# Kernel tuning notes

Hardware: AMD Instinct MI355X
Metric: run time of the kernel (lower is better)

Reference implementation:

```python
import jax, jax.numpy as jnp
import numpy as np

E = 8      # num_experts
K = 2      # top_k
D = 512    # model dim
H = 2048   # expert hidden dim (4*dim)
EPS = 1e-6


def _rmsnorm(x, w):
    # x: [..., H], w broadcastable to x
    return x * jax.lax.rsqrt(jnp.mean(x * x, axis=-1, keepdims=True) + EPS) * w


def setup_inputs() -> dict:
    key = jax.random.key(0)
    ks = jax.random.split(key, 5)
    B, T = 4, 2048
    x = jax.random.normal(ks[0], (B, T, D), dtype=jnp.float32)
    gate_w = jax.random.normal(ks[1], (D, E), dtype=jnp.float32) / np.sqrt(D)
    w1 = jax.random.normal(ks[2], (E, D, H), dtype=jnp.float32) / np.sqrt(D)
    w2 = jax.random.normal(ks[3], (E, H, H), dtype=jnp.float32) / np.sqrt(H)
    w3 = jax.random.normal(ks[4], (E, H, D), dtype=jnp.float32) / np.sqrt(H)
    n1 = jnp.ones((E, H), dtype=jnp.float32)
    n2 = jnp.ones((E, H), dtype=jnp.float32)
    return {"x": x, "gate_w": gate_w, "w1": w1, "w2": w2, "w3": w3, "n1": n1, "n2": n2}


def reference(x, gate_w, w1, w2, w3, n1, n2):
    B, T, Dm = x.shape
    xf = x.reshape(-1, Dm)                              # [N, D]
    logits = xf @ gate_w                                # [N, E]
    tk_logits, tk_idx = jax.lax.top_k(logits, K)        # [N, K]
    gates = jax.nn.softmax(tk_logits, axis=-1)          # [N, K]

    # Dense compute of all experts (naive MoE, as in the original module).
    h1 = jax.nn.gelu(jnp.einsum('nd,edh->enh', xf, w1), approximate=False)
    h1 = _rmsnorm(h1, n1[:, None, :])                   # [E, N, H]
    h2 = jax.nn.gelu(jnp.einsum('enh,ehk->enk', h1, w2), approximate=False)
    h2 = _rmsnorm(h2, n2[:, None, :])                   # [E, N, H]
    # dropout is identity in eval mode
    expert_out = jnp.einsum('enh,ehd->ned', h2 + h1, w3)  # [N, E, D]

    sel = jnp.take_along_axis(expert_out, tk_idx[:, :, None], axis=1)  # [N, K, D]
    out = jnp.sum(gates[:, :, None] * sel, axis=1)       # [N, D]
    return out.reshape(B, T, Dm)
```

## Files before the change

### kernel.cpp

```cpp
#include <hip/hip_runtime.h>
#include <hip/hip_bf16.h>

using bf16 = __hip_bfloat16;
using short8 = __attribute__((ext_vector_type(8))) short;
using float4v = __attribute__((ext_vector_type(4))) float;

#define N_TOK 8192
#define DMODEL 512
#define HDIM 2048
#define NEXP 8
#define NPAIR 16384
#define PAIR_PAD 16512
#define NGBLK 2048

#define ASYNC_CP16(gsrc, ldst)                                                   \
    __builtin_amdgcn_global_load_lds(                                            \
        (const __attribute__((address_space(1))) void*)(gsrc),                   \
        (__attribute__((address_space(3))) void*)(ldst), 16, 0, 0)

typedef __attribute__((address_space(3))) char lds3_t;

#define BAR() asm volatile("s_barrier" ::: "memory")
#define WAIT_VM4() asm volatile("s_waitcnt vmcnt(4)" ::: "memory")
#define WAIT_VM0() asm volatile("s_waitcnt vmcnt(0)" ::: "memory")
#define SBAR() __builtin_amdgcn_sched_barrier(0)
#define WAITL_(n) asm volatile("s_waitcnt lgkmcnt(" #n ")" ::: "memory")
#define WAITL(n) WAITL_(n)
#define DSR(dst, addr, imm) \
    asm volatile("ds_read_b128 %0, %1 offset:%2" : "=v"(dst) : "v"(addr), "i"(imm))

__device__ __forceinline__ float gelu_fast(float v) {
    float u = v * (0.7978845608f + 0.0356774081f * v * v);
    float t = __expf(-2.0f * u);
    return v * __builtin_amdgcn_rcpf(1.0f + t);
}
__device__ __forceinline__ float bf2f(short s) {
    return __uint_as_float(((unsigned)(unsigned short)s) << 16);
}
__device__ __forceinline__ short f2bf(float f) {
    return (short)__bfloat16_as_ushort(__float2bfloat16(f));
}

__global__ void cvt_x_k(const float* __restrict__ x, bf16* __restrict__ xb) {
    int i = blockIdx.x * 256 + threadIdx.x;
    if (i >= N_TOK * DMODEL / 4) return;
    const float4 f = *(const float4*)(x + (size_t)i * 4);
    union { ushort u[4]; uint2 v; } r;
    r.u[0] = __bfloat16_as_ushort(__float2bfloat16(f.x));
    r.u[1] = __bfloat16_as_ushort(__float2bfloat16(f.y));
    r.u[2] = __bfloat16_as_ushort(__float2bfloat16(f.z));
    r.u[3] = __bfloat16_as_ushort(__float2bfloat16(f.w));
    *(uint2*)(xb + (size_t)i * 4) = r.v;
}

__global__ void gating_k(const float* __restrict__ x, const float* __restrict__ gw,
                         int* __restrict__ tok_idx, float* __restrict__ tok_gate,
                         int* __restrict__ blkc) {
    __shared__ int hist[8];
    if (threadIdx.x < 8) hist[threadIdx.x] = 0;
    __syncthreads();
    int n = blockIdx.x * 4 + (threadIdx.x >> 6);
    int lane = threadIdx.x & 63;
    double acc[NEXP];
#pragma unroll
    for (int e = 0; e < NEXP; e++) acc[e] = 0.0;
    const float* xr = x + (size_t)n * DMODEL;
    for (int d = lane; d < DMODEL; d += 64) {
        float xv = xr[d];
        const float* g = gw + (size_t)d * NEXP;
#pragma unroll
        for (int e = 0; e < NEXP; e++) acc[e] += (double)xv * (double)g[e];
    }
#pragma unroll
    for (int m = 32; m >= 1; m >>= 1)
#pragma unroll
        for (int e = 0; e < NEXP; e++) acc[e] += __shfl_xor(acc[e], m, 64);
    if (lane == 0) {
        double best = acc[0]; int bi = 0;
#pragma unroll
        for (int e = 1; e < NEXP; e++) if (acc[e] > best) { best = acc[e]; bi = e; }
        double best2 = -1e300; int bi2 = 0;
#pragma unroll
        for (int e = 0; e < NEXP; e++) if (e != bi && acc[e] > best2) { best2 = acc[e]; bi2 = e; }
        double t = exp(best2 - best);
        float g0 = (float)(1.0 / (1.0 + t));
        float g1 = (float)(t / (1.0 + t));
        tok_idx[2 * n] = bi;  tok_idx[2 * n + 1] = bi2;
        tok_gate[2 * n] = g0; tok_gate[2 * n + 1] = g1;
        atomicAdd(&hist[bi], 1);
        atomicAdd(&hist[bi2], 1);
    }
    __syncthreads();
    if (threadIdx.x < 8) blkc[blockIdx.x * 8 + threadIdx.x] = hist[threadIdx.x];
}

__global__ void scan_k(const int* __restrict__ blkc, int* __restrict__ blkbase,
                       int* __restrict__ offs_g) {
    __shared__ int totals[8];
    const int tid = threadIdx.x;
    const int w = tid >> 6, l = tid & 63;
    int loc[32];
    int s = 0;
#pragma unroll
    for (int i = 0; i < 32; i++) { loc[i] = blkc[(size_t)(l * 32 + i) * 8 + w]; s += loc[i]; }
    int inc = s;
#pragma unroll
    for (int d = 1; d < 64; d <<= 1) {
        int v = __shfl_up(inc, d, 64);
        if (l >= d) inc += v;
    }
    const int excl = inc - s;
    if (l == 63) totals[w] = inc;
    __syncthreads();
    int off = 0;
#pragma unroll
    for (int e = 0; e < 8; e++) off += (e < w) ? totals[e] : 0;
    int run = off + excl;
#pragma unroll
    for (int i = 0; i < 32; i++) { blkbase[(size_t)(l * 32 + i) * 8 + w] = run; run += loc[i]; }
    if (tid < 9) {
        int o = 0;
        for (int e = 0; e < tid; e++) o += totals[e];
        offs_g[tid] = o;
    }
}

__global__ void place_k(const int* __restrict__ tok_idx, const float* __restrict__ tok_gate,
                        const int* __restrict__ blkbase,
                        int* __restrict__ pair_token, float* __restrict__ pair_gate,
                        int* __restrict__ pair_expert, int* __restrict__ pair_of) {
    const int p = blockIdx.x * 256 + threadIdx.x;
    const int lane = threadIdx.x & 63;
    const int e = tok_idx[p];
    const unsigned long long below = (1ull << lane) - 1ull;
    const unsigned long long grpmask = 0xFFull << (lane & 56);
    int rank = 0;
#pragma unroll
    for (int v = 0; v < 8; v++) {
        unsigned long long bal = __ballot(e == v);
        if (e == v) rank = (int)__popcll(bal & grpmask & below);
    }
    const int b = p >> 3;
    const int s = blkbase[b * 8 + e] + rank;
    pair_token[s] = p >> 1;
    pair_gate[s] = tok_gate[p];
    pair_expert[s] = e;
    pair_of[p] = s;
}

__global__ void transpose_all_k(const float* __restrict__ w1, const float* __restrict__ w2,
                                const float* __restrict__ w3, bf16* __restrict__ w1t,
                                bf16* __restrict__ w2t, bf16* __restrict__ w3t) {
    int bid = blockIdx.x;
    int e = bid / 1536, r = bid % 1536;
    const float* W; bf16* Wt; int K, N, kt, nt;
    if (r < 256)       { W = w1; Wt = w1t; K = 512;  N = 2048; kt = r & 7;  nt = r >> 3; }
    else if (r < 1280) { r -= 256;  W = w2; Wt = w2t; K = 2048; N = 2048; kt = r & 31; nt = r >> 5; }
    else               { r -= 1280; W = w3; Wt = w3t; K = 2048; N = 512;  kt = r & 31; nt = r >> 5; }
    const float* Wp = W + (size_t)e * K * N;
    bf16* Wtp = Wt + (size_t)e * K * N;
    int k0 = kt * 64, n0 = nt * 64;
    __shared__ float tile[64][65];
    int t = threadIdx.x;
    int kr = t >> 4, nc = (t & 15) * 4;
#pragma unroll
    for (int j = 0; j < 4; j++) {
        float4 f = *(const float4*)&Wp[(size_t)(k0 + kr + j * 16) * N + n0 + nc];
        tile[kr + j * 16][nc]     = f.x;
        tile[kr + j * 16][nc + 1] = f.y;
        tile[kr + j * 16][nc + 2] = f.z;
        tile[kr + j * 16][nc + 3] = f.w;
    }
    __syncthreads();
    int n = t >> 2, kc = (t & 3) * 4;
#pragma unroll
    for (int j = 0; j < 4; j++) {
        int k = j * 16 + kc;
        union { ushort u[4]; uint2 v; } rr;
#pragma unroll
        for (int i = 0; i < 4; i++)
            rr.u[i] = __bfloat16_as_ushort(__float2bfloat16(tile[k + i][n]));
        *(uint2*)&Wtp[(size_t)(n0 + n) * K + k0 + k] = rr.v;
    }
}

template <int KD, int ND, int EPI>
__launch_bounds__(512, 2)
__global__ void gemm256_k(const bf16* __restrict__ Abase, const bf16* __restrict__ Bt,
                          const int* __restrict__ row_map, const int* __restrict__ offs,
                          bf16* __restrict__ Hout, float* __restrict__ Yout,
                          const float* __restrict__ pair_gate) {
    constexpr int NB = ND / 256;
    const int bid = blockIdx.x;
    const int e = bid & 7;
    const int j = bid >> 3;
    const int mb = j / NB, nb = j % NB;
    const int off = offs[e];
    const int cnt = offs[e + 1] - off;
    const int m0 = mb * 256;
    if (m0 >= cnt) return;
    const int n0 = nb * 256;

    __shared__ __align__(16) char LDS[131072];

    const int tid = threadIdx.x;
    const int lane = tid & 63, w = tid >> 6;
    const int wm = w >> 2, wn = w & 3;
    const int c16 = lane & 15, q = lane >> 4;
    const bf16* Bp = Bt + (size_t)e * ND * KD;

    const unsigned s0 = (unsigned)((q ^ (lane & 7)) << 4);
    const unsigned a_rd = (unsigned)((wm * 128 + c16) * 128) + s0;
    const unsigned b_rd = 32768u + (unsigned)((wn * 64 + c16) * 128) + s0;

    const int dstA = w * 4096;
    const int srow = w * 32 + (lane >> 3);
    const int kperm = ((lane & 7) ^ (lane >> 3)) << 3;
    const bf16* pa[4]; const bf16* pb[4];
#pragma unroll
    for (int jj = 0; jj < 4; jj++) {
        int rl = m0 + srow + jj * 8;
        if (rl > cnt - 1) rl = cnt - 1;
        size_t ga = row_map ? (size_t)row_map[off + rl] : (size_t)(off + rl);
        pa[jj] = Abase + ga * KD + kperm;
        pb[jj] = Bp + (size_t)(n0 + srow + jj * 8) * KD + kperm;
    }

    float4v acc[8][4];
#pragma unroll
    for (int mi = 0; mi < 8; mi++)
#pragma unroll
        for (int ni = 0; ni < 4; ni++) acc[mi][ni] = (float4v){0.f, 0.f, 0.f, 0.f};

    lds3_t* L3 = (lds3_t*)LDS;
    constexpr int NT = KD / 64;

#define MFMA_ROW(mi_)                                                     \
    _Pragma("unroll") for (int ni = 0; ni < 4; ni++)                      \
        acc[mi_][ni] = __builtin_amdgcn_mfma_f32_16x16x32_bf16(           \
            af[mi_], bq[ni], acc[mi_][ni], 0, 0, 0);

#define PHASE_PIPE(AB, BB)                                                \
    DSR(bq[0], BB, 0);       DSR(bq[1], BB, 2048);                        \
    DSR(bq[2], BB, 4096);    DSR(bq[3], BB, 6144);                        \
    DSR(af[0], AB, 0);       DSR(af[1], AB, 2048);                        \
    DSR(af[2], AB, 4096);                                                 \
    WAITL(2); SBAR();                                                     \
    __builtin_amdgcn_s_setprio(1);                                        \
    DSR(af[3], AB, 6144);   MFMA_ROW(0); WAITL(2); SBAR();                \
    DSR(af[4], AB, 8192);   MFMA_ROW(1); WAITL(2); SBAR();                \
    DSR(af[5], AB, 10240);  MFMA_ROW(2); WAITL(2); SBAR();                \
    DSR(af[6], AB, 12288);  MFMA_ROW(3); WAITL(2); SBAR();                \
    DSR(af[7], AB, 14336);  MFMA_ROW(4); WAITL(2); SBAR();                \
    MFMA_ROW(5); WAITL(1); SBAR();                                        \
    MFMA_ROW(6); WAITL(0); SBAR();                                        \
    MFMA_ROW(7);                                                          \
    __builtin_amdgcn_s_setprio(0);                                        \
    SBAR();

#pragma unroll
    for (int jj = 0; jj < 4; jj++) { ASYNC_CP16(pa[jj], LDS + dstA + jj * 1024); pa[jj] += 64; }
#pragma unroll
    for (int jj = 0; jj < 4; jj++) { ASYNC_CP16(pb[jj], LDS + 32768 + dstA + jj * 1024); pb[jj] += 64; }
    SBAR();

    unsigned cur = 0;
    for (int tt = 0; tt < NT; ++tt) {
        short8 af[8], bq[4];
        const bool pf = (tt + 1 < NT);
        BAR();
        if (pf) {
            const unsigned nbuf = cur ^ 65536u;
            SBAR();
#pragma unroll
            for (int jj = 0; jj < 4; jj++) { ASYNC_CP16(pa[jj], LDS + nbuf + dstA + jj * 1024); pa[jj] += 64; }
            SBAR();
            WAIT_VM4();
        } else {
            WAIT_VM0();
        }
        SBAR();
        BAR();
        {
            lds3_t* AB = L3 + (a_rd + cur);
            lds3_t* BB = L3 + (b_rd + cur);
            PHASE_PIPE(AB, BB);
        }
        if (pf) {
            const unsigned nbuf = cur ^ 65536u;
            SBAR();
#pragma unroll
            for (int jj = 0; jj < 4; jj++) { ASYNC_CP16(pb[jj], LDS + nbuf + 32768 + dstA + jj * 1024); pb[jj] += 64; }
            SBAR();
        }
        {
            lds3_t* AB = L3 + ((a_rd + cur) ^ 0x40u);
            lds3_t* BB = L3 + ((b_rd + cur) ^ 0x40u);
            PHASE_PIPE(AB, BB);
        }
        cur ^= 65536u;
    }
#undef PHASE_PIPE
#undef MFMA_ROW

#pragma unroll
    for (int mi = 0; mi < 8; mi++)
#pragma unroll
        for (int reg = 0; reg < 4; reg++) {
            int row = wm * 128 + mi * 16 + q * 4 + reg;
            if (m0 + row < cnt) {
                size_t gp = (size_t)(off + m0 + row);
                if (EPI == 0) {
#pragma unroll
                    for (int ni = 0; ni < 4; ni++) {
                        int col = n0 + wn * 64 + ni * 16 + c16;
                        Hout[gp * ND + col] = __float2bfloat16(gelu_fast(acc[mi][ni][reg]));
                    }
                } else {
                    float gt = pair_gate[gp];
#pragma unroll
                    for (int ni = 0; ni < 4; ni++) {
                        int col = n0 + wn * 64 + ni * 16 + c16;
                        Yout[gp * ND + col] = acc[mi][ni][reg] * gt;
                    }
                }
            }
        }
}

template <int KD, int ND, int EPI>
__launch_bounds__(256, 2)
__global__ void gemm_moe_k(const bf16* __restrict__ Abase, const bf16* __restrict__ Bt,
                           const int* __restrict__ row_map, const int* __restrict__ offs,
                           bf16* __restrict__ Hout, float* __restrict__ Yout,
                           const float* __restrict__ pair_gate) {
    constexpr int NB = ND / 128;
    const int bid = blockIdx.x;
    const int e = bid & 7;
    const int j = bid >> 3;
    const int mb = j / NB, nb = j % NB;
    const int off = offs[e];
    const int cnt = offs[e + 1] - off;
    const int m0 = mb * 128;
    if (m0 >= cnt) return;
    const int n0 = nb * 128;

    __shared__ alignas(16) bf16 As[128 * 32];
    __shared__ alignas(16) bf16 Bs[128 * 32];

    const int t = threadIdx.x;
    const int lane = t & 63, w = t >> 6;
    const bf16* Bp = Bt + (size_t)e * ND * KD;

    const int i0 = 2 * w, i1 = 2 * w + 1;
    const int ar0 = i0 * 16 + (lane >> 2);
    const int ar1 = i1 * 16 + (lane >> 2);
    const int kc = (lane & 3) * 8;

    size_t ga0, ga1;
    if (row_map) {
        ga0 = (m0 + ar0 < cnt) ? (size_t)row_map[off + m0 + ar0] : 0;
        ga1 = (m0 + ar1 < cnt) ? (size_t)row_map[off + m0 + ar1] : 0;
    } else {
        ga0 = (size_t)(off + m0 + ar0);
        ga1 = (size_t)(off + m0 + ar1);
    }
    const bf16* Ap0 = Abase + ga0 * KD + kc;
    const bf16* Ap1 = Abase + ga1 * KD + kc;
    const bf16* Bq0 = Bp + (size_t)(n0 + ar0) * KD + kc;
    const bf16* Bq1 = Bp + (size_t)(n0 + ar1) * KD + kc;

    bf16* lA0 = As + i0 * 512;
    bf16* lA1 = As + i1 * 512;
    bf16* lB0 = Bs + i0 * 512;
    bf16* lB1 = Bs + i1 * 512;

    const int wm = (w >> 1) * 64, wn = (w & 1) * 64;
    const int q = lane >> 4, c16 = lane & 15;

    float4v acc[4][4];
#pragma unroll
    for (int mi = 0; mi < 4; mi++)
#pragma unroll
        for (int ni = 0; ni < 4; ni++) acc[mi][ni] = (float4v){0.f, 0.f, 0.f, 0.f};

    for (int k0 = 0; k0 < KD; k0 += 32) {
        ASYNC_CP16(Ap0 + k0, lA0);
        ASYNC_CP16(Ap1 + k0, lA1);
        ASYNC_CP16(Bq0 + k0, lB0);
        ASYNC_CP16(Bq1 + k0, lB1);
        __syncthreads();
        short8 af[4], bfr[4];
#pragma unroll
        for (int mi = 0; mi < 4; mi++)
            af[mi] = *(const short8*)&As[(wm + mi * 16 + c16) * 32 + q * 8];
#pragma unroll
        for (int ni = 0; ni < 4; ni++)
            bfr[ni] = *(const short8*)&Bs[(wn + ni * 16 + c16) * 32 + q * 8];
#pragma unroll
        for (int mi = 0; mi < 4; mi++)
#pragma unroll
            for (int ni = 0; ni < 4; ni++)
                acc[mi][ni] = __builtin_amdgcn_mfma_f32_16x16x32_bf16(
                    af[mi], bfr[ni], acc[mi][ni], 0, 0, 0);
        __syncthreads();
    }

#pragma unroll
    for (int mi = 0; mi < 4; mi++)
#pragma unroll
        for (int reg = 0; reg < 4; reg++) {
            int row = wm + mi * 16 + q * 4 + reg;
            if (m0 + row < cnt) {
                size_t gp = (size_t)(off + m0 + row);
                if (EPI == 0) {
#pragma unroll
                    for (int ni = 0; ni < 4; ni++) {
                        int col = n0 + wn + ni * 16 + c16;
                        Hout[gp * ND + col] = __float2bfloat16(gelu_fast(acc[mi][ni][reg]));
                    }
                } else {
                    float gt = pair_gate[gp];
#pragma unroll
                    for (int ni = 0; ni < 4; ni++) {
                        int col = n0 + wn + ni * 16 + c16;
                        Yout[gp * ND + col] = acc[mi][ni][reg] * gt;
                    }
                }
            }
        }
}

template <int ADD>
__global__ void rmsnorm_k(bf16* __restrict__ H, const bf16* __restrict__ H1n,
                          const float* __restrict__ nw, const int* __restrict__ pair_expert) {
    int p = blockIdx.x;
    int t = threadIdx.x;
    bf16* row = H + (size_t)p * HDIM + t * 8;
    short8 hv = *(const short8*)row;
    float v[8];
    float ss = 0.f;
#pragma unroll
    for (int i = 0; i < 8; i++) {
        v[i] = bf2f(hv[i]);
        ss += v[i] * v[i];
    }
#pragma unroll
    for (int m = 32; m >= 1; m >>= 1) ss += __shfl_xor(ss, m, 64);
    __shared__ float s4[4];
    int wv = t >> 6, lane = t & 63;
    if (lane == 0) s4[wv] = ss;
    __syncthreads();
    ss = s4[0] + s4[1] + s4[2] + s4[3];
    float scale = rsqrtf(ss / (float)HDIM + 1e-6f);
    int e = pair_expert[p];
    const float* nr = nw + (size_t)e * HDIM + t * 8;
    float4 na = *(const float4*)nr;
    float4 nb = *(const float4*)(nr + 4);
    float nv[8] = {na.x, na.y, na.z, na.w, nb.x, nb.y, nb.z, nb.w};
    short8 res;
    short8 r8;
    if (ADD) r8 = *(const short8*)(H1n + (size_t)p * HDIM + t * 8);
#pragma unroll
    for (int i = 0; i < 8; i++) {
        float o = v[i] * scale * nv[i];
        if (ADD) o += bf2f(r8[i]);
        res[i] = f2bf(o);
    }
    *(short8*)row = res;
}

__global__ void combine_k(const float* __restrict__ y, const int* __restrict__ pair_of,
                          float* __restrict__ out) {
    int i = blockIdx.x * 256 + threadIdx.x;
    if (i >= N_TOK * DMODEL / 4) return;
    int n = i >> 7, d4 = (i & 127) << 2;
    int p0 = pair_of[2 * n], p1 = pair_of[2 * n + 1];
    const float4 a = *(const float4*)(y + (size_t)p0 * DMODEL + d4);
    const float4 b = *(const float4*)(y + (size_t)p1 * DMODEL + d4);
    float4 r;
    r.x = a.x + b.x; r.y = a.y + b.y; r.z = a.z + b.z; r.w = a.w + b.w;
    *(float4*)(out + (size_t)n * DMODEL + d4) = r;
}

extern "C" void kernel_launch(void* const* d_in, const int* in_sizes, int n_in,
                              void* d_out, int out_size, void* d_ws, size_t ws_size,
                              hipStream_t stream) {
    const float* x  = (const float*)d_in[0];
    const float* gw = (const float*)d_in[1];
    const float* w1 = (const float*)d_in[2];
    const float* w2 = (const float*)d_in[3];
    const float* w3 = (const float*)d_in[4];
    const float* n1 = (const float*)d_in[5];
    const float* n2 = (const float*)d_in[6];
    float* out = (float*)d_out;

    char* wsp = (char*)d_ws;
    size_t cur = 0;
    auto take = [&](size_t bytes) -> void* {
        void* p = wsp + cur;
        cur += (bytes + 255) & ~(size_t)255;
        return p;
    };
    bf16* xb  = (bf16*)take((size_t)N_TOK * DMODEL * 2);
    bf16* w1t = (bf16*)take((size_t)NEXP * DMODEL * HDIM * 2);
    bf16* w2t = (bf16*)take((size_t)NEXP * HDIM * HDIM * 2);
    bf16* w3t = (bf16*)take((size_t)NEXP * HDIM * DMODEL * 2);
    bf16* h1  = (bf16*)take((size_t)PAIR_PAD * HDIM * 2);
    bf16* h2  = (bf16*)take((size_t)PAIR_PAD * HDIM * 2);
    float* y  = (float*)take((size_t)PAIR_PAD * DMODEL * 4);
    int* tok_idx     = (int*)take((size_t)NPAIR * 4);
    float* tok_gate  = (float*)take((size_t)NPAIR * 4);
    int* pair_token  = (int*)take((size_t)PAIR_PAD * 4);
    float* pair_gate = (float*)take((size_t)PAIR_PAD * 4);
    int* pair_expert = (int*)take((size_t)PAIR_PAD * 4);
    int* pair_of     = (int*)take((size_t)NPAIR * 4);
    int* blkc    = (int*)take((size_t)NGBLK * 8 * 4);
    int* blkbase = (int*)take((size_t)NGBLK * 8 * 4);
    int* offs    = (int*)take((NEXP + 1) * 4);

    cvt_x_k<<<N_TOK * DMODEL / 4 / 256, 256, 0, stream>>>(x, xb);
    gating_k<<<NGBLK, 256, 0, stream>>>(x, gw, tok_idx, tok_gate, blkc);
    scan_k<<<1, 512, 0, stream>>>(blkc, blkbase, offs);
    place_k<<<NPAIR / 256, 256, 0, stream>>>(tok_idx, tok_gate, blkbase,
                                             pair_token, pair_gate, pair_expert, pair_of);

    transpose_all_k<<<NEXP * 1536, 256, 0, stream>>>(w1, w2, w3, w1t, w2t, w3t);

    gemm256_k<DMODEL, HDIM, 0><<<NEXP * 64 * (HDIM / 256), 512, 0, stream>>>(
        xb, w1t, pair_token, offs, h1, nullptr, nullptr);
    rmsnorm_k<0><<<NPAIR, 256, 0, stream>>>(h1, nullptr, n1, pair_expert);

    gemm256_k<HDIM, HDIM, 0><<<NEXP * 64 * (HDIM / 256), 512, 0, stream>>>(
        h1, w2t, nullptr, offs, h2, nullptr, nullptr);
    rmsnorm_k<1><<<NPAIR, 256, 0, stream>>>(h2, h1, n2, pair_expert);

    gemm_moe_k<HDIM, DMODEL, 1><<<NEXP * 64 * (DMODEL / 128), 256, 0, stream>>>(
        h2, w3t, nullptr, offs, nullptr, y, pair_gate);

    combine_k<<<N_TOK * DMODEL / 4 / 256, 256, 0, stream>>>(y, pair_of, out);
}
```

Baseline: 653.0 us.

## Halve GEMM K-tile to 32 and split A/B loads across wave halves

Reduces the K step of the 256x256 grouped GEMM from 64 to 32, halving the double-buffered LDS footprint to 64KB, and changes the LDS swizzle and row stride to match. Waves 0-3 now load A while waves 4-7 load B, each with 4 async copies per stage, replacing the earlier scheme where every wave loaded both A and B. The aim is lower LDS use, which could let more blocks reside per CU, and simpler load issue. The cost is twice as many barrier and prefetch iterations per K, each covering less MFMA work.

After: 700.5 us. +7.3%, slower.

```diff
diff --git a/kernel.cpp b/kernel.cpp
--- a/kernel.cpp
+++ b/kernel.cpp
@@ -201,7 +201,7 @@
     if (m0 >= cnt) return;
     const int n0 = nb * 256;
 
-    __shared__ __align__(16) char LDS[131072];
+    __shared__ __align__(16) char LDS[65536];
 
     const int tid = threadIdx.x;
     const int lane = tid & 63, w = tid >> 6;
@@ -209,21 +209,27 @@
     const int c16 = lane & 15, q = lane >> 4;
     const bf16* Bp = Bt + (size_t)e * ND * KD;
 
-    const unsigned s0 = (unsigned)((q ^ (lane & 7)) << 4);
-    const unsigned a_rd = (unsigned)((wm * 128 + c16) * 128) + s0;
-    const unsigned b_rd = 32768u + (unsigned)((wn * 64 + c16) * 128) + s0;
-
-    const int dstA = w * 4096;
-    const int srow = w * 32 + (lane >> 3);
-    const int kperm = ((lane & 7) ^ (lane >> 3)) << 3;
-    const bf16* pa[4]; const bf16* pb[4];
+    const unsigned sw = (unsigned)((q ^ (c16 & 3)) << 4);
+    const unsigned a_rd = (unsigned)((wm * 128 + c16) * 64) + sw;
+    const unsigned b_rd = 16384u + (unsigned)((wn * 64 + c16) * 64) + sw;
+
+    const int wmod = w & 3;
+    const bool isB = (w >= 4);
+    const int dst0 = (isB ? 16384 : 0) + wmod * 4096;
+    const int srow0 = wmod * 64 + (lane >> 2);
+    const int kperm = ((lane & 3) ^ ((lane >> 2) & 3)) << 3;
+    const bf16* ps[4];
 #pragma unroll
     for (int jj = 0; jj < 4; jj++) {
-        int rl = m0 + srow + jj * 8;
-        if (rl > cnt - 1) rl = cnt - 1;
-        size_t ga = row_map ? (size_t)row_map[off + rl] : (size_t)(off + rl);
-        pa[jj] = Abase + ga * KD + kperm;
-        pb[jj] = Bp + (size_t)(n0 + srow + jj * 8) * KD + kperm;
+        int r = srow0 + jj * 16;
+        if (!isB) {
+            int rl = m0 + r;
+            if (rl > cnt - 1) rl = cnt - 1;
+            size_t ga = row_map ? (size_t)row_map[off + rl] : (size_t)(off + rl);
+            ps[jj] = Abase + ga * KD + kperm;
+        } else {
+            ps[jj] = Bp + (size_t)(n0 + r) * KD + kperm;
+        }
     }
 
     float4v acc[8][4];
@@ -233,7 +239,7 @@
         for (int ni = 0; ni < 4; ni++) acc[mi][ni] = (float4v){0.f, 0.f, 0.f, 0.f};
 
     lds3_t* L3 = (lds3_t*)LDS;
-    constexpr int NT = KD / 64;
+    constexpr int NT = KD / 32;
 
 #define MFMA_ROW(mi_)                                                     \
     _Pragma("unroll") for (int ni = 0; ni < 4; ni++)                      \
@@ -241,17 +247,17 @@
             af[mi_], bq[ni], acc[mi_][ni], 0, 0, 0);
 
 #define PHASE_PIPE(AB, BB)                                                \
-    DSR(bq[0], BB, 0);       DSR(bq[1], BB, 2048);                        \
-    DSR(bq[2], BB, 4096);    DSR(bq[3], BB, 6144);                        \
-    DSR(af[0], AB, 0);       DSR(af[1], AB, 2048);                        \
-    DSR(af[2], AB, 4096);                                                 \
+    DSR(bq[0], BB, 0);       DSR(bq[1], BB, 1024);                        \
+    DSR(bq[2], BB, 2048);    DSR(bq[3], BB, 3072);                        \
+    DSR(af[0], AB, 0);       DSR(af[1], AB, 1024);                        \
+    DSR(af[2], AB, 2048);                                                 \
     WAITL(2); SBAR();                                                     \
     __builtin_amdgcn_s_setprio(1);                                        \
-    DSR(af[3], AB, 6144);   MFMA_ROW(0); WAITL(2); SBAR();                \
-    DSR(af[4], AB, 8192);   MFMA_ROW(1); WAITL(2); SBAR();                \
-    DSR(af[5], AB, 10240);  MFMA_ROW(2); WAITL(2); SBAR();                \
-    DSR(af[6], AB, 12288);  MFMA_ROW(3); WAITL(2); SBAR();                \
-    DSR(af[7], AB, 14336);  MFMA_ROW(4); WAITL(2); SBAR();                \
+    DSR(af[3], AB, 3072);   MFMA_ROW(0); WAITL(2); SBAR();                \
+    DSR(af[4], AB, 4096);   MFMA_ROW(1); WAITL(2); SBAR();                \
+    DSR(af[5], AB, 5120);   MFMA_ROW(2); WAITL(2); SBAR();                \
+    DSR(af[6], AB, 6144);   MFMA_ROW(3); WAITL(2); SBAR();                \
+    DSR(af[7], AB, 7168);   MFMA_ROW(4); WAITL(2); SBAR();                \
     MFMA_ROW(5); WAITL(1); SBAR();                                        \
     MFMA_ROW(6); WAITL(0); SBAR();                                        \
     MFMA_ROW(7);                                                          \
@@ -259,9 +265,7 @@
     SBAR();
 
 #pragma unroll
-    for (int jj = 0; jj < 4; jj++) { ASYNC_CP16(pa[jj], LDS + dstA + jj * 1024); pa[jj] += 64; }
-#pragma unroll
-    for (int jj = 0; jj < 4; jj++) { ASYNC_CP16(pb[jj], LDS + 32768 + dstA + jj * 1024); pb[jj] += 64; }
+    for (int jj = 0; jj < 4; jj++) { ASYNC_CP16(ps[jj], LDS + dst0 + jj * 1024); ps[jj] += 32; }
     SBAR();
 
     unsigned cur = 0;
@@ -270,10 +274,10 @@
         const bool pf = (tt + 1 < NT);
         BAR();
         if (pf) {
-            const unsigned nbuf = cur ^ 65536u;
+            const unsigned nbuf = cur ^ 32768u;
             SBAR();
 #pragma unroll
-            for (int jj = 0; jj < 4; jj++) { ASYNC_CP16(pa[jj], LDS + nbuf + dstA + jj * 1024); pa[jj] += 64; }
+            for (int jj = 0; jj < 4; jj++) { ASYNC_CP16(ps[jj], LDS + nbuf + dst0 + jj * 1024); ps[jj] += 32; }
             SBAR();
             WAIT_VM4();
         } else {
@@ -286,19 +290,7 @@
             lds3_t* BB = L3 + (b_rd + cur);
             PHASE_PIPE(AB, BB);
         }
-        if (pf) {
-            const unsigned nbuf = cur ^ 65536u;
-            SBAR();
-#pragma unroll
-            for (int jj = 0; jj < 4; jj++) { ASYNC_CP16(pb[jj], LDS + nbuf + 32768 + dstA + jj * 1024); pb[jj] += 64; }
-            SBAR();
-        }
-        {
-            lds3_t* AB = L3 + ((a_rd + cur) ^ 0x40u);
-            lds3_t* BB = L3 + ((b_rd + cur) ^ 0x40u);
-            PHASE_PIPE(AB, BB);
-        }
-        cur ^= 65536u;
+        cur ^= 32768u;
     }
 #undef PHASE_PIPE
 #undef MFMA_ROW
```
